# Performance work log

Hardware: AMD Instinct MI355X
Metric: run time of the kernel (lower is better)

## Reference

```python
import jax, jax.numpy as jnp
import numpy as np

N, E, G = 50000, 1600000, 64
D_IN, D_EDGE, D_H, D_U, D_OUT = 32, 32, 64, 16, 32


def _linear_params(key, d_in, d_out):
    kw, kb = jax.random.split(key)
    lim = 1.0 / np.sqrt(d_in)
    W = jax.random.uniform(kw, (d_in, d_out), minval=-lim, maxval=lim, dtype=jnp.float32)
    b = jax.random.uniform(kb, (d_out,), minval=-lim, maxval=lim, dtype=jnp.float32)
    return W, b


def setup_inputs() -> dict:
    key = jax.random.key(0)
    ks = jax.random.split(key, 10)
    x = jax.random.normal(ks[0], (N, D_IN), dtype=jnp.float32)
    edge_index = jax.random.randint(ks[1], (2, E), 0, N, dtype=jnp.int64)
    edge_attr = jax.random.normal(ks[2], (E, D_EDGE), dtype=jnp.float32)
    u = jax.random.normal(ks[3], (G, D_U), dtype=jnp.float32)
    batch = jnp.sort(jax.random.randint(ks[4], (N,), 0, G, dtype=jnp.int64))
    W1a, b1a = _linear_params(ks[5], D_IN + D_EDGE, D_H)   # node linear 0
    W1b, b1b = _linear_params(ks[6], D_H, D_H)             # node linear 1 (hidden)
    W2a, b2a = _linear_params(ks[7], D_IN + D_H + D_U, D_H)
    W2b, b2b = _linear_params(ks[8], D_H, D_OUT)
    return dict(x=x, edge_index=edge_index, edge_attr=edge_attr, u=u, batch=batch,
                W1a=W1a, b1a=b1a, W1b=W1b, b1b=b1b,
                W2a=W2a, b2a=b2a, W2b=W2b, b2b=b2b)


def reference(x, edge_index, edge_attr, u, batch,
              W1a, b1a, W1b, b1b, W2a, b2a, W2b, b2b):
    row, col = edge_index[0], edge_index[1]
    # edge-level MLP on [x[col] || edge_attr]
    h = jnp.concatenate([x[col], edge_attr], axis=1)          # [E, D_IN+D_EDGE]
    h = jax.nn.relu(h @ W1a + b1a)                            # [E, D_H]
    h = jax.nn.relu(h @ W1b + b1b)                            # [E, D_H]
    # scatter_mean over destination nodes (row), dim_size = N
    summed = jax.ops.segment_sum(h, row, num_segments=N)      # [N, D_H]
    counts = jax.ops.segment_sum(jnp.ones((h.shape[0],), h.dtype), row, num_segments=N)
    agg = summed / jnp.maximum(counts, 1.0)[:, None]
    # node-level MLP on [x || agg || u[batch]]
    z = jnp.concatenate([x, agg, u[batch]], axis=1)           # [N, D_IN+D_H+D_U]
    z = jax.nn.relu(z @ W2a + b2a)
    return z @ W2b + b2b                                      # [N, D_OUT]
```

## Files before the change

kernel.cpp:

```cpp
#include <hip/hip_runtime.h>
#include <hip/hip_bf16.h>


typedef __attribute__((ext_vector_type(8))) short bf16x8;
typedef __attribute__((ext_vector_type(4))) float f32x4;

__device__ __forceinline__ unsigned short f2bf(float f) {
    __bf16 h = (__bf16)f;
    unsigned short u;
    __builtin_memcpy(&u, &h, 2);
    return u;
}
__device__ __forceinline__ bf16x8 pack8(const float4 a, const float4 b) {
    bf16x8 c;
    c[0] = (short)f2bf(a.x); c[1] = (short)f2bf(a.y);
    c[2] = (short)f2bf(a.z); c[3] = (short)f2bf(a.w);
    c[4] = (short)f2bf(b.x); c[5] = (short)f2bf(b.y);
    c[6] = (short)f2bf(b.z); c[7] = (short)f2bf(b.w);
    return c;
}


__global__ __launch_bounds__(256) void count_rows_convx(
    const int* __restrict__ erow, int* __restrict__ counts, int E,
    const float* __restrict__ x, unsigned short* __restrict__ xbf, int nx8)
{
    const int gid = blockIdx.x * blockDim.x + threadIdx.x;
    const int stride = gridDim.x * blockDim.x;
    for (int i = gid; i < nx8; i += stride) {
        const float4 a = ((const float4*)x)[2 * i];
        const float4 b = ((const float4*)x)[2 * i + 1];
        *(bf16x8*)(xbf + (size_t)i * 8) = pack8(a, b);
    }
    const int n4 = E >> 2;
    for (int i = gid; i < n4; i += stride) {
        const int4 r = ((const int4*)erow)[i];
        atomicAdd(&counts[r.x], 1);
        atomicAdd(&counts[r.y], 1);
        atomicAdd(&counts[r.z], 1);
        atomicAdd(&counts[r.w], 1);
    }
    for (int i = (n4 << 2) + gid; i < E; i += stride)
        atomicAdd(&counts[erow[i]], 1);
}

__global__ __launch_bounds__(256) void scan_blocks(
    const int* __restrict__ counts, int* __restrict__ excl,
    int* __restrict__ bsum, int N)
{
    __shared__ int tmp[256];
    const int t = threadIdx.x;
    const int i = blockIdx.x * 256 + t;
    const int v = (i < N) ? counts[i] : 0;
    tmp[t] = v; __syncthreads();
#pragma unroll
    for (int o = 1; o < 256; o <<= 1) {
        const int a = (t >= o) ? tmp[t - o] : 0;
        __syncthreads();
        tmp[t] += a;
        __syncthreads();
    }
    if (i < N) excl[i] = tmp[t] - v;
    if (t == 255) bsum[blockIdx.x] = tmp[t];
}

__global__ __launch_bounds__(256) void scan_bsum(int* __restrict__ bsum, int nb)
{
    __shared__ int tmp[256];
    const int t = threadIdx.x;
    const int v = (t < nb) ? bsum[t] : 0;
    tmp[t] = v; __syncthreads();
#pragma unroll
    for (int o = 1; o < 256; o <<= 1) {
        const int a = (t >= o) ? tmp[t - o] : 0;
        __syncthreads();
        tmp[t] += a;
        __syncthreads();
    }
    if (t < nb) bsum[t] = tmp[t] - v;
}

__global__ __launch_bounds__(256) void scan_add(
    int* __restrict__ rowstart, int* __restrict__ cursor,
    const int* __restrict__ bsum, int N, int E)
{
    const int i = blockIdx.x * 256 + threadIdx.x;
    if (i < N) {
        const int v = rowstart[i] + bsum[blockIdx.x];
        rowstart[i] = v;
        cursor[i]   = v;
    }
    if (i == 0) rowstart[N] = E;
}

__global__ __launch_bounds__(256) void permute_conv(
    const int* __restrict__ erow, const int* __restrict__ ecol,
    const float* __restrict__ eattr,
    int* __restrict__ cursor, int* __restrict__ sorted1,
    unsigned short* __restrict__ eattr_s, int E)
{
    const int gid = blockIdx.x * blockDim.x + threadIdx.x;
    const int stride = gridDim.x * blockDim.x;
    for (int i = gid; i < E; i += stride) {
        const int r = erow[i];
        const int c = ecol[i];
        const int pos = atomicAdd(&cursor[r], 1);
        sorted1[pos] = (int)((unsigned)c | ((unsigned)r << 16));
        const float4* src = (const float4*)(eattr + (size_t)i * 32);
        unsigned short* dst = eattr_s + (size_t)pos * 32;
#pragma unroll
        for (int q = 0; q < 4; ++q)
            *(bf16x8*)(dst + 8 * q) = pack8(src[2 * q], src[2 * q + 1]);
    }
}

__global__ __launch_bounds__(256) void permute_edges(
    const int* __restrict__ erow, const int* __restrict__ ecol,
    int* __restrict__ cursor, int2* __restrict__ sorted2, int E)
{
    const int gid = blockIdx.x * blockDim.x + threadIdx.x;
    const int stride = gridDim.x * blockDim.x;
    const int n4 = E >> 2;
    for (int i = gid; i < n4; i += stride) {
        const int4 r = ((const int4*)erow)[i];
        const int4 c = ((const int4*)ecol)[i];
        const int e0 = i << 2;
        int pos;
        pos = atomicAdd(&cursor[r.x], 1);
        sorted2[pos] = int2{e0,     (int)((unsigned)c.x | ((unsigned)r.x << 16))};
        pos = atomicAdd(&cursor[r.y], 1);
        sorted2[pos] = int2{e0 + 1, (int)((unsigned)c.y | ((unsigned)r.y << 16))};
        pos = atomicAdd(&cursor[r.z], 1);
        sorted2[pos] = int2{e0 + 2, (int)((unsigned)c.z | ((unsigned)r.z << 16))};
        pos = atomicAdd(&cursor[r.w], 1);
        sorted2[pos] = int2{e0 + 3, (int)((unsigned)c.w | ((unsigned)r.w << 16))};
    }
    for (int i = (n4 << 2) + gid; i < E; i += stride) {
        const int r = erow[i];
        const int pos = atomicAdd(&cursor[r], 1);
        sorted2[pos] = int2{i, (int)((unsigned)ecol[i] | ((unsigned)r << 16))};
    }
}


__global__ __launch_bounds__(256, 3) void edge_mlp_v2(
    const unsigned short* __restrict__ xbf,
    const int*            __restrict__ sorted1,
    const unsigned short* __restrict__ eattr_s,
    const float* __restrict__ W1a,  const float* __restrict__ b1a,
    const float* __restrict__ W1b,  const float* __restrict__ b1b,
    float* __restrict__ summed, int E)
{
    __shared__ __align__(16) unsigned short H2[4 * 16 * 64];

    const int tid  = threadIdx.x;
    const int lane = tid & 63;
    const int wv   = tid >> 6;
    const int g    = lane >> 4;
    const int el   = lane & 15;

    unsigned short* const h2w = H2 + wv * (16 * 64);

    bf16x8 wa[4][2], wb[4][2];
    f32x4  bias1[4];
    float  bias2s[4];
#pragma unroll
    for (int mt = 0; mt < 4; ++mt) {
        const int o = mt * 16 + el;
#pragma unroll
        for (int ks = 0; ks < 2; ++ks) {
            bf16x8 ta, tb;
#pragma unroll
            for (int j = 0; j < 8; ++j) {
                const int k = ks * 32 + 8 * g + j;
                ta[j] = (short)f2bf(W1a[k * 64 + o]);
                tb[j] = (short)f2bf(W1b[k * 64 + o]);
            }
            wa[mt][ks] = ta;
            wb[mt][ks] = tb;
        }
#pragma unroll
        for (int r = 0; r < 4; ++r) bias1[mt][r] = b1a[mt * 16 + 4 * g + r];
        bias2s[mt] = b1b[o];
    }

    const int ntile = (E + 15) >> 4;
    const int wid   = blockIdx.x * 4 + wv;
    const int nw    = gridDim.x * 4;
    const int sw    = el & 7;

    for (int t = wid; t < ntile; t += nw) {
        const int ebase = t << 4;
        const int e     = ebase + el;

        int row, col;
        if (e < E) {
            const int m = sorted1[e];
            row = (int)((unsigned)m >> 16);
            col = m & 0xFFFF;
        } else { row = -1; col = 0; }

        const int ee = (e < E) ? e : (E - 1);
        const bf16x8 bf0 = *(const bf16x8*)(xbf + (size_t)col * 32 + 8 * g);
        const bf16x8 bf1 = *(const bf16x8*)(eattr_s + (size_t)ee * 32 + 8 * g);

        f32x4 a0 = bias1[0], a1 = bias1[1], a2 = bias1[2], a3 = bias1[3];
        a0 = __builtin_amdgcn_mfma_f32_16x16x32_bf16(wa[0][0], bf0, a0, 0, 0, 0);
        a1 = __builtin_amdgcn_mfma_f32_16x16x32_bf16(wa[1][0], bf0, a1, 0, 0, 0);
        a2 = __builtin_amdgcn_mfma_f32_16x16x32_bf16(wa[2][0], bf0, a2, 0, 0, 0);
        a3 = __builtin_amdgcn_mfma_f32_16x16x32_bf16(wa[3][0], bf0, a3, 0, 0, 0);
        a0 = __builtin_amdgcn_mfma_f32_16x16x32_bf16(wa[0][1], bf1, a0, 0, 0, 0);
        a1 = __builtin_amdgcn_mfma_f32_16x16x32_bf16(wa[1][1], bf1, a1, 0, 0, 0);
        a2 = __builtin_amdgcn_mfma_f32_16x16x32_bf16(wa[2][1], bf1, a2, 0, 0, 0);
        a3 = __builtin_amdgcn_mfma_f32_16x16x32_bf16(wa[3][1], bf1, a3, 0, 0, 0);

        unsigned short* hrow = h2w + el * 64;
        {
            f32x4 accs[4] = {a0, a1, a2, a3};
#pragma unroll
            for (int mt = 0; mt < 4; ++mt) {
                unsigned short pk[4];
#pragma unroll
                for (int r = 0; r < 4; ++r) pk[r] = f2bf(fmaxf(accs[mt][r], 0.f));
                const int hid   = mt * 16 + 4 * g;
                const int chunk = hid >> 3;
                const int off   = hid & 7;
                *(uint2*)(hrow + ((chunk ^ sw) * 8 + off)) = *(uint2*)pk;
            }
        }

        const bf16x8 hb0 = *(const bf16x8*)(hrow + (((0 + g) ^ sw) * 8));
        const bf16x8 hb1 = *(const bf16x8*)(hrow + (((4 + g) ^ sw) * 8));
        f32x4 d0 = {bias2s[0], bias2s[0], bias2s[0], bias2s[0]};
        f32x4 d1 = {bias2s[1], bias2s[1], bias2s[1], bias2s[1]};
        f32x4 d2 = {bias2s[2], bias2s[2], bias2s[2], bias2s[2]};
        f32x4 d3 = {bias2s[3], bias2s[3], bias2s[3], bias2s[3]};
        d0 = __builtin_amdgcn_mfma_f32_16x16x32_bf16(hb0, wb[0][0], d0, 0, 0, 0);
        d1 = __builtin_amdgcn_mfma_f32_16x16x32_bf16(hb0, wb[1][0], d1, 0, 0, 0);
        d2 = __builtin_amdgcn_mfma_f32_16x16x32_bf16(hb0, wb[2][0], d2, 0, 0, 0);
        d3 = __builtin_amdgcn_mfma_f32_16x16x32_bf16(hb0, wb[3][0], d3, 0, 0, 0);
        d0 = __builtin_amdgcn_mfma_f32_16x16x32_bf16(hb1, wb[0][1], d0, 0, 0, 0);
        d1 = __builtin_amdgcn_mfma_f32_16x16x32_bf16(hb1, wb[1][1], d1, 0, 0, 0);
        d2 = __builtin_amdgcn_mfma_f32_16x16x32_bf16(hb1, wb[2][1], d2, 0, 0, 0);
        d3 = __builtin_amdgcn_mfma_f32_16x16x32_bf16(hb1, wb[3][1], d3, 0, 0, 0);

#pragma unroll
        for (int r = 0; r < 4; ++r) {
            d0[r] = fmaxf(d0[r], 0.f);
            d1[r] = fmaxf(d1[r], 0.f);
            d2[r] = fmaxf(d2[r], 0.f);
            d3[r] = fmaxf(d3[r], 0.f);
        }

        const int prevrow = __shfl(row, lane - 1);
        unsigned long long bmask =
            __ballot((g == 0) && (el > 0) && (row != prevrow));
        bmask = (bmask & 0xFFFEull) | 0x10000ull;

        int s = 0;
        while (s < 16) {
            const int e2 = s + 1 + (__ffsll(bmask >> (s + 1)) - 1);
            const int rowid = __shfl(row, s);
            if (rowid >= 0) {
                float s0 = 0.f, s1 = 0.f, s2v = 0.f, s3 = 0.f;
#pragma unroll
                for (int r = 0; r < 4; ++r) {
                    const int ej = 4 * g + r;
                    const bool in = (ej >= s) && (ej < e2);
                    s0  += in ? d0[r] : 0.f;
                    s1  += in ? d1[r] : 0.f;
                    s2v += in ? d2[r] : 0.f;
                    s3  += in ? d3[r] : 0.f;
                }
                s0  += __shfl_xor(s0, 16);  s0  += __shfl_xor(s0, 32);
                s1  += __shfl_xor(s1, 16);  s1  += __shfl_xor(s1, 32);
                s2v += __shfl_xor(s2v, 16); s2v += __shfl_xor(s2v, 32);
                s3  += __shfl_xor(s3, 16);  s3  += __shfl_xor(s3, 32);
                const float val = (g == 0) ? s0 : (g == 1) ? s1
                                : (g == 2) ? s2v : s3;
                unsafeAtomicAdd(&summed[(size_t)rowid * 64 + lane], val);
            }
            s = e2;
        }
    }
}


__global__ __launch_bounds__(256, 3) void edge_mlp_mfma(
    const float* __restrict__ x,
    const int2*  __restrict__ sorted2,
    const float* __restrict__ eattr,
    const float* __restrict__ W1a,  const float* __restrict__ b1a,
    const float* __restrict__ W1b,  const float* __restrict__ b1b,
    float* __restrict__ summed, int E)
{
    __shared__ __align__(16) unsigned short H2[4 * 16 * 64];
    const int tid  = threadIdx.x;
    const int lane = tid & 63;
    const int wv   = tid >> 6;
    const int g    = lane >> 4;
    const int el   = lane & 15;
    unsigned short* const h2w = H2 + wv * (16 * 64);

    bf16x8 wa[4][2], wb[4][2];
    f32x4  bias1[4];
    float  bias2s[4];
#pragma unroll
    for (int mt = 0; mt < 4; ++mt) {
        const int o = mt * 16 + el;
#pragma unroll
        for (int ks = 0; ks < 2; ++ks) {
            bf16x8 ta, tb;
#pragma unroll
            for (int j = 0; j < 8; ++j) {
                const int k = ks * 32 + 8 * g + j;
                ta[j] = (short)f2bf(W1a[k * 64 + o]);
                tb[j] = (short)f2bf(W1b[k * 64 + o]);
            }
            wa[mt][ks] = ta;
            wb[mt][ks] = tb;
        }
#pragma unroll
        for (int r = 0; r < 4; ++r) bias1[mt][r] = b1a[mt * 16 + 4 * g + r];
        bias2s[mt] = b1b[o];
    }

    const int ntile = (E + 15) >> 4;
    const int wid   = blockIdx.x * 4 + wv;
    const int nw    = gridDim.x * 4;
    const int sw    = el & 7;

    for (int t = wid; t < ntile; t += nw) {
        const int ebase = t << 4;
        int2 s2; int row;
        if (ebase + el < E) {
            s2 = sorted2[ebase + el];
            row = (int)((unsigned)s2.y >> 16);
        } else { s2 = int2{0, 0}; row = -1; }

        bf16x8 bf0, bf1;
        {
            const float4* xp = (const float4*)(x + (size_t)(s2.y & 0xFFFF) * 32 + 8 * g);
            const float4* ap = (const float4*)(eattr + (size_t)s2.x * 32 + 8 * g);
            bf0 = pack8(xp[0], xp[1]);
            bf1 = pack8(ap[0], ap[1]);
        }

        f32x4 a0 = bias1[0], a1 = bias1[1], a2 = bias1[2], a3 = bias1[3];
        a0 = __builtin_amdgcn_mfma_f32_16x16x32_bf16(wa[0][0], bf0, a0, 0, 0, 0);
        a1 = __builtin_amdgcn_mfma_f32_16x16x32_bf16(wa[1][0], bf0, a1, 0, 0, 0);
        a2 = __builtin_amdgcn_mfma_f32_16x16x32_bf16(wa[2][0], bf0, a2, 0, 0, 0);
        a3 = __builtin_amdgcn_mfma_f32_16x16x32_bf16(wa[3][0], bf0, a3, 0, 0, 0);
        a0 = __builtin_amdgcn_mfma_f32_16x16x32_bf16(wa[0][1], bf1, a0, 0, 0, 0);
        a1 = __builtin_amdgcn_mfma_f32_16x16x32_bf16(wa[1][1], bf1, a1, 0, 0, 0);
        a2 = __builtin_amdgcn_mfma_f32_16x16x32_bf16(wa[2][1], bf1, a2, 0, 0, 0);
        a3 = __builtin_amdgcn_mfma_f32_16x16x32_bf16(wa[3][1], bf1, a3, 0, 0, 0);

        unsigned short* hrow = h2w + el * 64;
        {
            f32x4 accs[4] = {a0, a1, a2, a3};
#pragma unroll
            for (int mt = 0; mt < 4; ++mt) {
                unsigned short pk[4];
#pragma unroll
                for (int r = 0; r < 4; ++r) pk[r] = f2bf(fmaxf(accs[mt][r], 0.f));
                const int hid   = mt * 16 + 4 * g;
                const int chunk = hid >> 3;
                const int off   = hid & 7;
                *(uint2*)(hrow + ((chunk ^ sw) * 8 + off)) = *(uint2*)pk;
            }
        }

        const bf16x8 hb0 = *(const bf16x8*)(hrow + (((0 + g) ^ sw) * 8));
        const bf16x8 hb1 = *(const bf16x8*)(hrow + (((4 + g) ^ sw) * 8));
        f32x4 d0 = {bias2s[0], bias2s[0], bias2s[0], bias2s[0]};
        f32x4 d1 = {bias2s[1], bias2s[1], bias2s[1], bias2s[1]};
        f32x4 d2 = {bias2s[2], bias2s[2], bias2s[2], bias2s[2]};
        f32x4 d3 = {bias2s[3], bias2s[3], bias2s[3], bias2s[3]};
        d0 = __builtin_amdgcn_mfma_f32_16x16x32_bf16(hb0, wb[0][0], d0, 0, 0, 0);
        d1 = __builtin_amdgcn_mfma_f32_16x16x32_bf16(hb0, wb[1][0], d1, 0, 0, 0);
        d2 = __builtin_amdgcn_mfma_f32_16x16x32_bf16(hb0, wb[2][0], d2, 0, 0, 0);
        d3 = __builtin_amdgcn_mfma_f32_16x16x32_bf16(hb0, wb[3][0], d3, 0, 0, 0);
        d0 = __builtin_amdgcn_mfma_f32_16x16x32_bf16(hb1, wb[0][1], d0, 0, 0, 0);
        d1 = __builtin_amdgcn_mfma_f32_16x16x32_bf16(hb1, wb[1][1], d1, 0, 0, 0);
        d2 = __builtin_amdgcn_mfma_f32_16x16x32_bf16(hb1, wb[2][1], d2, 0, 0, 0);
        d3 = __builtin_amdgcn_mfma_f32_16x16x32_bf16(hb1, wb[3][1], d3, 0, 0, 0);

#pragma unroll
        for (int r = 0; r < 4; ++r) {
            d0[r] = fmaxf(d0[r], 0.f);
            d1[r] = fmaxf(d1[r], 0.f);
            d2[r] = fmaxf(d2[r], 0.f);
            d3[r] = fmaxf(d3[r], 0.f);
        }

        const int prevrow = __shfl(row, lane - 1);
        unsigned long long bmask =
            __ballot((g == 0) && (el > 0) && (row != prevrow));
        bmask = (bmask & 0xFFFEull) | 0x10000ull;

        int s = 0;
        while (s < 16) {
            const int e = s + 1 + (__ffsll(bmask >> (s + 1)) - 1);
            const int rowid = __shfl(row, s);
            if (rowid >= 0) {
                float s0 = 0.f, s1 = 0.f, s2v = 0.f, s3 = 0.f;
#pragma unroll
                for (int r = 0; r < 4; ++r) {
                    const int ej = 4 * g + r;
                    const bool in = (ej >= s) && (ej < e);
                    s0  += in ? d0[r] : 0.f;
                    s1  += in ? d1[r] : 0.f;
                    s2v += in ? d2[r] : 0.f;
                    s3  += in ? d3[r] : 0.f;
                }
                s0  += __shfl_xor(s0, 16);  s0  += __shfl_xor(s0, 32);
                s1  += __shfl_xor(s1, 16);  s1  += __shfl_xor(s1, 32);
                s2v += __shfl_xor(s2v, 16); s2v += __shfl_xor(s2v, 32);
                s3  += __shfl_xor(s3, 16);  s3  += __shfl_xor(s3, 32);
                const float val = (g == 0) ? s0 : (g == 1) ? s1
                                : (g == 2) ? s2v : s3;
                unsafeAtomicAdd(&summed[(size_t)rowid * 64 + lane], val);
            }
            s = e;
        }
    }
}


__global__ __launch_bounds__(256, 2) void node_mlp_mfma(
    const float* __restrict__ x,
    const float* __restrict__ summed,
    const int*   __restrict__ rowstart,
    const float* __restrict__ u,
    const int*   __restrict__ batch,
    const float* __restrict__ W2a,
    const float* __restrict__ b2a,
    const float* __restrict__ W2b,
    const float* __restrict__ b2b,
    float* __restrict__ out,
    int N)
{
    __shared__ __align__(16) unsigned short In[64 * 128];
    __shared__ __align__(16) unsigned short H[64 * 64];

    const int tid  = threadIdx.x;
    const int lane = tid & 63;
    const int wv   = tid >> 6;
    const int g    = lane >> 4;
    const int el   = lane & 15;

    bf16x8 wa[4][4];
    f32x4  bias1[4];
#pragma unroll
    for (int mt = 0; mt < 4; ++mt) {
        const int o = mt * 16 + el;
#pragma unroll
        for (int ks = 0; ks < 4; ++ks) {
            bf16x8 ta;
#pragma unroll
            for (int j = 0; j < 8; ++j) {
                const int k = ks * 32 + 8 * g + j;
                ta[j] = (k < 112) ? (short)f2bf(W2a[k * 64 + o]) : (short)0;
            }
            wa[mt][ks] = ta;
        }
#pragma unroll
        for (int r = 0; r < 4; ++r) bias1[mt][r] = b2a[mt * 16 + 4 * g + r];
    }
    bf16x8 wb[2][2];
    float  bias2s[2];
#pragma unroll
    for (int nt = 0; nt < 2; ++nt) {
        const int o = nt * 16 + el;
#pragma unroll
        for (int ks = 0; ks < 2; ++ks) {
            bf16x8 tb;
#pragma unroll
            for (int j = 0; j < 8; ++j) {
                const int k = ks * 32 + 8 * g + j;
                tb[j] = (short)f2bf(W2b[k * 32 + o]);
            }
            wb[nt][ks] = tb;
        }
        bias2s[nt] = b2b[o];
    }

    unsigned short* const inrow = In + (wv * 16) * 128;
    unsigned short* const hrow0 = H + (wv * 16) * 64;

    const int ntile = (N + 15) >> 4;
    const int wid   = blockIdx.x * 4 + wv;
    const int nw    = gridDim.x * 4;

    for (int t = wid; t < ntile; t += nw) {
        const int nbase = t << 4;
        {
            const int le = lane >> 2;
            const int p  = lane & 3;
            const int n  = nbase + le;
            float4 v[8];
            if (n < N) {
                if (p == 0) {
                    const float4* xp = (const float4*)(x + (size_t)n * 32);
#pragma unroll
                    for (int q = 0; q < 8; ++q) v[q] = xp[q];
                } else if (p < 3) {
                    const int cnt = rowstart[n + 1] - rowstart[n];
                    const float inv = 1.0f / fmaxf((float)cnt, 1.0f);
                    const float4* sp = (const float4*)(summed + (size_t)n * 64 + (p - 1) * 32);
#pragma unroll
                    for (int q = 0; q < 8; ++q) {
                        v[q] = sp[q];
                        v[q].x *= inv; v[q].y *= inv; v[q].z *= inv; v[q].w *= inv;
                    }
                } else {
                    const int gb = batch[n];
                    const float4* up = (const float4*)(u + (size_t)gb * 16);
#pragma unroll
                    for (int q = 0; q < 4; ++q) v[q] = up[q];
#pragma unroll
                    for (int q = 4; q < 8; ++q) v[q] = float4{0.f, 0.f, 0.f, 0.f};
                }
            } else {
#pragma unroll
                for (int q = 0; q < 8; ++q) v[q] = float4{0.f, 0.f, 0.f, 0.f};
            }
            const int sw = le & 7;
            unsigned short* row = inrow + le * 128;
#pragma unroll
            for (int q = 0; q < 4; ++q) {
                const int cc = 4 * p + q;
                const int ci = (cc & 8) | ((cc & 7) ^ sw);
                *(bf16x8*)(row + ci * 8) = pack8(v[2 * q], v[2 * q + 1]);
            }
        }

        const unsigned short* brow = inrow + el * 128;
        const int sw7 = el & 7;
        f32x4 a0 = bias1[0], a1 = bias1[1], a2 = bias1[2], a3 = bias1[3];
#pragma unroll
        for (int ks = 0; ks < 4; ++ks) {
            const int cc = ks * 4 + g;
            const int ci = (cc & 8) | ((cc & 7) ^ sw7);
            const bf16x8 bf = *(const bf16x8*)(brow + ci * 8);
            a0 = __builtin_amdgcn_mfma_f32_16x16x32_bf16(wa[0][ks], bf, a0, 0, 0, 0);
            a1 = __builtin_amdgcn_mfma_f32_16x16x32_bf16(wa[1][ks], bf, a1, 0, 0, 0);
            a2 = __builtin_amdgcn_mfma_f32_16x16x32_bf16(wa[2][ks], bf, a2, 0, 0, 0);
            a3 = __builtin_amdgcn_mfma_f32_16x16x32_bf16(wa[3][ks], bf, a3, 0, 0, 0);
        }

        unsigned short* hrow = hrow0 + el * 64;
        {
            f32x4 accs[4] = {a0, a1, a2, a3};
#pragma unroll
            for (int mt = 0; mt < 4; ++mt) {
                unsigned short pk[4];
#pragma unroll
                for (int r = 0; r < 4; ++r) pk[r] = f2bf(fmaxf(accs[mt][r], 0.f));
                const int hid   = mt * 16 + 4 * g;
                const int chunk = hid >> 3;
                const int off   = hid & 7;
                *(uint2*)(hrow + ((chunk ^ sw7) * 8 + off)) = *(uint2*)pk;
            }
        }

        const bf16x8 hb0 = *(const bf16x8*)(hrow + (((0 + g) ^ sw7) * 8));
        const bf16x8 hb1 = *(const bf16x8*)(hrow + (((4 + g) ^ sw7) * 8));
        f32x4 dn0 = {bias2s[0], bias2s[0], bias2s[0], bias2s[0]};
        f32x4 dn1 = {bias2s[1], bias2s[1], bias2s[1], bias2s[1]};
        dn0 = __builtin_amdgcn_mfma_f32_16x16x32_bf16(hb0, wb[0][0], dn0, 0, 0, 0);
        dn1 = __builtin_amdgcn_mfma_f32_16x16x32_bf16(hb0, wb[1][0], dn1, 0, 0, 0);
        dn0 = __builtin_amdgcn_mfma_f32_16x16x32_bf16(hb1, wb[0][1], dn0, 0, 0, 0);
        dn1 = __builtin_amdgcn_mfma_f32_16x16x32_bf16(hb1, wb[1][1], dn1, 0, 0, 0);

        if (nbase + 16 <= N) {
#pragma unroll
            for (int r = 0; r < 4; ++r) {
                float* dst = out + (size_t)(nbase + 4 * g + r) * 32 + el;
                dst[0]  = dn0[r];
                dst[16] = dn1[r];
            }
        } else {
#pragma unroll
            for (int r = 0; r < 4; ++r) {
                const int n = nbase + 4 * g + r;
                if (n < N) {
                    float* dst = out + (size_t)n * 32 + el;
                    dst[0]  = dn0[r];
                    dst[16] = dn1[r];
                }
            }
        }
    }
}

extern "C" void kernel_launch(void* const* d_in, const int* in_sizes, int n_in,
                              void* d_out, int out_size, void* d_ws, size_t ws_size,
                              hipStream_t stream) {
    const float* x     = (const float*)d_in[0];
    const int*   eidx  = (const int*)d_in[1];
    const float* eattr = (const float*)d_in[2];
    const float* u     = (const float*)d_in[3];
    const int*   batch = (const int*)d_in[4];
    const float* W1a   = (const float*)d_in[5];
    const float* b1a   = (const float*)d_in[6];
    const float* W1b   = (const float*)d_in[7];
    const float* b1b   = (const float*)d_in[8];
    const float* W2a   = (const float*)d_in[9];
    const float* b2a   = (const float*)d_in[10];
    const float* W2b   = (const float*)d_in[11];
    const float* b2b   = (const float*)d_in[12];
    float* out = (float*)d_out;

    const int N = in_sizes[0] / 32;
    const int E = in_sizes[1] / 2;
    const int* erow = eidx;
    const int* ecol = eidx + E;
    const int nb = (N + 255) / 256;

    const size_t need_full = (size_t)E * 64 + (size_t)N * 64 + (size_t)E * 4
                           + (size_t)N * 256 + (size_t)(3 * N + 1) * 4 + 1024;

    if (ws_size >= need_full) {
        char* p = (char*)d_ws;
        unsigned short* eattr_s = (unsigned short*)p; p += (size_t)E * 64;
        unsigned short* xbf     = (unsigned short*)p; p += (size_t)N * 64;
        int*   sorted1  = (int*)p;   p += (size_t)E * 4;
        float* summed   = (float*)p; p += (size_t)N * 256;
        int*   counts   = (int*)p;   p += (size_t)N * 4;
        int*   rowstart = (int*)p;   p += (size_t)(N + 1) * 4;
        int*   cursor   = (int*)p;   p += (size_t)N * 4;
        int*   bsum     = (int*)p;

        hipMemsetAsync(summed, 0, (size_t)N * 256 + (size_t)N * 4, stream);
        count_rows_convx<<<1024, 256, 0, stream>>>(erow, counts, E, x, xbf, N * 4);
        scan_blocks<<<nb, 256, 0, stream>>>(counts, rowstart, bsum, N);
        scan_bsum<<<1, 256, 0, stream>>>(bsum, nb);
        scan_add<<<nb, 256, 0, stream>>>(rowstart, cursor, bsum, N, E);
        permute_conv<<<2048, 256, 0, stream>>>(erow, ecol, eattr, cursor,
                                               sorted1, eattr_s, E);
        edge_mlp_v2<<<4096, 256, 0, stream>>>(xbf, sorted1, eattr_s,
                                              W1a, b1a, W1b, b1b, summed, E);
        node_mlp_mfma<<<784, 256, 0, stream>>>(x, summed, rowstart, u, batch,
                                               W2a, b2a, W2b, b2b, out, N);
    } else {
        int2*  sorted2  = (int2*)d_ws;
        float* summed   = (float*)(sorted2 + E);
        int*   counts   = (int*)(summed + (size_t)N * 64);
        int*   rowstart = counts + N;
        int*   cursor   = rowstart + (N + 1);
        int*   bsum     = cursor + N;

        hipMemsetAsync(summed, 0, ((size_t)N * 64 + N) * sizeof(float), stream);
        count_rows_convx<<<1024, 256, 0, stream>>>(erow, counts, E, x, nullptr, 0);
        scan_blocks<<<nb, 256, 0, stream>>>(counts, rowstart, bsum, N);
        scan_bsum<<<1, 256, 0, stream>>>(bsum, nb);
        scan_add<<<nb, 256, 0, stream>>>(rowstart, cursor, bsum, N, E);
        permute_edges<<<1024, 256, 0, stream>>>(erow, ecol, cursor, sorted2, E);
        edge_mlp_mfma<<<4096, 256, 0, stream>>>(x, sorted2, eattr,
                                                W1a, b1a, W1b, b1b, summed, E);
        node_mlp_mfma<<<784, 256, 0, stream>>>(x, summed, rowstart, u, batch,
                                               W2a, b2a, W2b, b2b, out, N);
    }
}
```

Baseline: 318.6 us.

## Two-pass bucketed edge permutation and prefetch sorted edge indices in edge MLP

Replaces the single-pass counting-sort scatter with two passes. The first bins edges by row>>8 into coarse buckets. The second walks the binned list in order, places each edge at its final position and converts its attributes to bf16 there, so the writes to sorted1 and eattr_s land in a much narrower address range. This costs an extra E*8-byte intermediate buffer, an extra read and write pass, and atomics on 196 bucket counters, which will be heavily contended. The edge MLP also software-prefetches the next tile's packed row/col index, and the fallback permute_edges drops its int4-vectorised loop.

Measured after the change: 1.202 ms. +277.4%, slower.

```diff
diff --git a/kernel.cpp b/kernel.cpp
--- a/kernel.cpp
+++ b/kernel.cpp
@@ -82,6 +82,7 @@
 
 __global__ __launch_bounds__(256) void scan_add(
     int* __restrict__ rowstart, int* __restrict__ cursor,
+    int* __restrict__ bucket_cursor,
     const int* __restrict__ bsum, int N, int E)
 {
     const int i = blockIdx.x * 256 + threadIdx.x;
@@ -89,28 +90,45 @@
         const int v = rowstart[i] + bsum[blockIdx.x];
         rowstart[i] = v;
         cursor[i]   = v;
+        if ((i & 255) == 0) bucket_cursor[i >> 8] = v;
     }
     if (i == 0) rowstart[N] = E;
 }
 
-__global__ __launch_bounds__(256) void permute_conv(
+__global__ __launch_bounds__(256) void bin_edges(
     const int* __restrict__ erow, const int* __restrict__ ecol,
-    const float* __restrict__ eattr,
-    int* __restrict__ cursor, int* __restrict__ sorted1,
-    unsigned short* __restrict__ eattr_s, int E)
+    int* __restrict__ bucket_cursor, int2* __restrict__ binned, int E)
 {
     const int gid = blockIdx.x * blockDim.x + threadIdx.x;
     const int stride = gridDim.x * blockDim.x;
     for (int i = gid; i < E; i += stride) {
         const int r = erow[i];
         const int c = ecol[i];
-        const int pos = atomicAdd(&cursor[r], 1);
-        sorted1[pos] = (int)((unsigned)c | ((unsigned)r << 16));
-        const float4* src = (const float4*)(eattr + (size_t)i * 32);
+        const int q = atomicAdd(&bucket_cursor[r >> 8], 1);
+        binned[q] = int2{i, (int)((unsigned)c | ((unsigned)r << 16))};
+    }
+}
+
+__global__ __launch_bounds__(256) void permute_gather_conv(
+    const int2* __restrict__ binned, const float* __restrict__ eattr,
+    int* __restrict__ cursor, int* __restrict__ sorted1,
+    unsigned short* __restrict__ eattr_s, int E)
+{
+    const int gid = blockIdx.x * blockDim.x + threadIdx.x;
+    const int stride = gridDim.x * blockDim.x;
+    for (int p = gid; p < E; p += stride) {
+        const int2 m2 = binned[p];
+        const int row = (int)((unsigned)m2.y >> 16);
+        const int pos = atomicAdd(&cursor[row], 1);
+        sorted1[pos] = m2.y;
+        const float4* src = (const float4*)(eattr + (size_t)m2.x * 32);
         unsigned short* dst = eattr_s + (size_t)pos * 32;
-#pragma unroll
-        for (int q = 0; q < 4; ++q)
-            *(bf16x8*)(dst + 8 * q) = pack8(src[2 * q], src[2 * q + 1]);
+        float4 v0 = src[0], v1 = src[1], v2 = src[2], v3 = src[3];
+        float4 v4 = src[4], v5 = src[5], v6 = src[6], v7 = src[7];
+        *(bf16x8*)(dst +  0) = pack8(v0, v1);
+        *(bf16x8*)(dst +  8) = pack8(v2, v3);
+        *(bf16x8*)(dst + 16) = pack8(v4, v5);
+        *(bf16x8*)(dst + 24) = pack8(v6, v7);
     }
 }
 
@@ -120,22 +138,7 @@
 {
     const int gid = blockIdx.x * blockDim.x + threadIdx.x;
     const int stride = gridDim.x * blockDim.x;
-    const int n4 = E >> 2;
-    for (int i = gid; i < n4; i += stride) {
-        const int4 r = ((const int4*)erow)[i];
-        const int4 c = ((const int4*)ecol)[i];
-        const int e0 = i << 2;
-        int pos;
-        pos = atomicAdd(&cursor[r.x], 1);
-        sorted2[pos] = int2{e0,     (int)((unsigned)c.x | ((unsigned)r.x << 16))};
-        pos = atomicAdd(&cursor[r.y], 1);
-        sorted2[pos] = int2{e0 + 1, (int)((unsigned)c.y | ((unsigned)r.y << 16))};
-        pos = atomicAdd(&cursor[r.z], 1);
-        sorted2[pos] = int2{e0 + 2, (int)((unsigned)c.z | ((unsigned)r.z << 16))};
-        pos = atomicAdd(&cursor[r.w], 1);
-        sorted2[pos] = int2{e0 + 3, (int)((unsigned)c.w | ((unsigned)r.w << 16))};
-    }
-    for (int i = (n4 << 2) + gid; i < E; i += stride) {
+    for (int i = gid; i < E; i += stride) {
         const int r = erow[i];
         const int pos = atomicAdd(&cursor[r], 1);
         sorted2[pos] = int2{i, (int)((unsigned)ecol[i] | ((unsigned)r << 16))};
@@ -189,16 +192,24 @@
     const int nw    = gridDim.x * 4;
     const int sw    = el & 7;
 
+    int m_cur;
+    {
+        const int e0 = (wid << 4) + el;
+        m_cur = sorted1[(e0 < E) ? e0 : 0];
+    }
+
     for (int t = wid; t < ntile; t += nw) {
         const int ebase = t << 4;
         const int e     = ebase + el;
 
-        int row, col;
-        if (e < E) {
-            const int m = sorted1[e];
-            row = (int)((unsigned)m >> 16);
-            col = m & 0xFFFF;
-        } else { row = -1; col = 0; }
+        const int m   = m_cur;
+        const int row = (e < E) ? (int)((unsigned)m >> 16) : -1;
+        const int col = (e < E) ? (m & 0xFFFF) : 0;
+
+        {
+            const int e2 = ((t + nw) << 4) + el;
+            m_cur = sorted1[(e2 < E) ? e2 : 0];
+        }
 
         const int ee = (e < E) ? e : (E - 1);
         const bf16x8 bf0 = *(const bf16x8*)(xbf + (size_t)col * 32 + 8 * g);
@@ -619,27 +630,32 @@
     const int* ecol = eidx + E;
     const int nb = (N + 255) / 256;
 
-    const size_t need_full = (size_t)E * 64 + (size_t)N * 64 + (size_t)E * 4
-                           + (size_t)N * 256 + (size_t)(3 * N + 1) * 4 + 1024;
+    const size_t need_full = (size_t)E * 64 + (size_t)N * 64 + (size_t)E * 8
+                           + (size_t)E * 4 + (size_t)N * 256
+                           + (size_t)(3 * N + 1) * 4 + 2048;
 
     if (ws_size >= need_full) {
         char* p = (char*)d_ws;
         unsigned short* eattr_s = (unsigned short*)p; p += (size_t)E * 64;
         unsigned short* xbf     = (unsigned short*)p; p += (size_t)N * 64;
+        int2*  binned   = (int2*)p;  p += (size_t)E * 8;
         int*   sorted1  = (int*)p;   p += (size_t)E * 4;
         float* summed   = (float*)p; p += (size_t)N * 256;
         int*   counts   = (int*)p;   p += (size_t)N * 4;
         int*   rowstart = (int*)p;   p += (size_t)(N + 1) * 4;
         int*   cursor   = (int*)p;   p += (size_t)N * 4;
+        int*   bucket_cursor = (int*)p; p += 1024;
         int*   bsum     = (int*)p;
 
         hipMemsetAsync(summed, 0, (size_t)N * 256 + (size_t)N * 4, stream);
         count_rows_convx<<<1024, 256, 0, stream>>>(erow, counts, E, x, xbf, N * 4);
         scan_blocks<<<nb, 256, 0, stream>>>(counts, rowstart, bsum, N);
         scan_bsum<<<1, 256, 0, stream>>>(bsum, nb);
-        scan_add<<<nb, 256, 0, stream>>>(rowstart, cursor, bsum, N, E);
-        permute_conv<<<2048, 256, 0, stream>>>(erow, ecol, eattr, cursor,
-                                               sorted1, eattr_s, E);
+        scan_add<<<nb, 256, 0, stream>>>(rowstart, cursor, bucket_cursor,
+                                         bsum, N, E);
+        bin_edges<<<1024, 256, 0, stream>>>(erow, ecol, bucket_cursor, binned, E);
+        permute_gather_conv<<<512, 256, 0, stream>>>(binned, eattr, cursor,
+                                                     sorted1, eattr_s, E);
         edge_mlp_v2<<<4096, 256, 0, stream>>>(xbf, sorted1, eattr_s,
                                               W1a, b1a, W1b, b1b, summed, E);
         node_mlp_mfma<<<784, 256, 0, stream>>>(x, summed, rowstart, u, batch,
@@ -650,13 +666,15 @@
         int*   counts   = (int*)(summed + (size_t)N * 64);
         int*   rowstart = counts + N;
         int*   cursor   = rowstart + (N + 1);
-        int*   bsum     = cursor + N;
+        int*   bucket_cursor = cursor + N;
+        int*   bsum     = bucket_cursor + 256;
 
         hipMemsetAsync(summed, 0, ((size_t)N * 64 + N) * sizeof(float), stream);
         count_rows_convx<<<1024, 256, 0, stream>>>(erow, counts, E, x, nullptr, 0);
         scan_blocks<<<nb, 256, 0, stream>>>(counts, rowstart, bsum, N);
         scan_bsum<<<1, 256, 0, stream>>>(bsum, nb);
-        scan_add<<<nb, 256, 0, stream>>>(rowstart, cursor, bsum, N, E);
+        scan_add<<<nb, 256, 0, stream>>>(rowstart, cursor, bucket_cursor,
+                                         bsum, N, E);
         permute_edges<<<1024, 256, 0, stream>>>(erow, ecol, cursor, sorted2, E);
         edge_mlp_mfma<<<4096, 256, 0, stream>>>(x, sorted2, eattr,
                                                 W1a, b1a, W1b, b1b, summed, E);
```
